# Performance work log

Hardware: AMD Instinct MI355X
Metric: run time of the kernel (lower is better)

## Reference

```python
import jax, jax.numpy as jnp
import numpy as np

DELTA = 1e-6  # small constant used throughout the original repo


def _theta(memory, keys):
    # batchwise cosine similarity: memory [b,m,w], keys [b,r,w] -> [b,r,m]
    a = memory / (jnp.linalg.norm(memory, axis=2, keepdims=True) + DELTA)
    b = keys / (jnp.linalg.norm(keys, axis=2, keepdims=True) + DELTA)
    return jnp.einsum('bmw,brw->brm', a, b)


def _content_weightings(memory, keys, strengths):
    d = _theta(memory, keys)                       # [b,r,m]
    s = jax.nn.softplus(strengths)[..., None]      # [b,r,1]
    return jax.nn.softmax(d * s, axis=2)


def _allocate(usage):
    # usage [b,m]
    u = DELTA + (1.0 - DELTA) * usage
    phi = jnp.argsort(u, axis=1)                          # ascending, like topk(largest=False)
    sorted_u = jnp.take_along_axis(u, phi, axis=1)
    sorted_alloc = (1.0 - sorted_u) * jnp.cumprod(sorted_u, axis=1)  # fake_cumprod == inclusive cumprod
    alloc = jnp.take_along_axis(sorted_alloc, phi, axis=1)           # faithful to .gather(1, phi) in source
    return alloc[:, None, :]                              # [b,1,m]


def _dnc_step(xi, W, bW, memory, link_matrix, precedence, read_weights, write_weights, usage_vector):
    b, m, w = memory.shape
    r = read_weights.shape[1]
    iface = xi @ W + bW                                   # [b, r*w + 3*w + 5*r + 3]
    i0 = r * w
    read_keys = iface[:, :i0].reshape(b, r, w)
    read_strengths = 1.0 + jax.nn.relu(iface[:, i0:i0 + r])              # [b,r]
    write_key = iface[:, i0 + r:i0 + r + w].reshape(b, 1, w)
    write_strength = (1.0 + jax.nn.relu(iface[:, i0 + r + w]))[:, None]  # [b,1]
    erase_vector = jax.nn.sigmoid(iface[:, i0 + r + w + 1:i0 + r + 2 * w + 1]).reshape(b, 1, w)
    write_vector = iface[:, i0 + r + 2 * w + 1:i0 + r + 3 * w + 1].reshape(b, 1, w)
    free_gates = jax.nn.sigmoid(iface[:, i0 + r + 3 * w + 1:i0 + 2 * r + 3 * w + 1])  # [b,r]
    allocation_gate = jax.nn.sigmoid(iface[:, i0 + 2 * r + 3 * w + 1])[:, None]       # [b,1]
    write_gate = jax.nn.sigmoid(iface[:, i0 + 2 * r + 3 * w + 2])[:, None]            # [b,1]
    # NOTE: source slices read_modes starting at the write_gate index (faithful) and softmaxes over dim 1
    read_modes = jax.nn.softmax(iface[:, i0 + 2 * r + 3 * w + 2:i0 + 5 * r + 3 * w + 2].reshape(b, r, 3), axis=1)

    # ---- write path ----
    usage = usage_vector + (1.0 - usage_vector) * (1.0 - jnp.prod(1.0 - write_weights, axis=1))
    psi = jnp.prod(1.0 - free_gates[:, :, None] * read_weights, axis=1)  # [b,m]
    usage = usage * psi

    write_content_w = _content_weightings(memory, write_key, write_strength)  # [b,1,m]
    alloc = _allocate(usage)                                                  # [b,1,m]
    ag = allocation_gate[:, :, None]
    wg = write_gate[:, :, None]
    new_write_w = wg * (ag * alloc + (1.0 - ag) * write_content_w)            # [b,1,m]

    weighted_resets = new_write_w[:, :, :, None] * erase_vector[:, :, None, :]  # [b,1,m,w]
    reset_gate = jnp.prod(1.0 - weighted_resets, axis=1)                        # [b,m,w]
    new_memory = memory * reset_gate + jnp.einsum('bkm,bkw->bmw', new_write_w, write_vector)

    prec4 = precedence[:, :, None, :]            # [b,1,1,m]
    ww_i = new_write_w[:, :, :, None]            # [b,1,m,1]
    ww_j = new_write_w[:, :, None, :]            # [b,1,1,m]
    new_link = (1.0 - ww_i - ww_j) * link_matrix + ww_i * prec4
    new_link = new_link * (1.0 - jnp.eye(m, dtype=memory.dtype))[None, None]

    new_prec = (1.0 - jnp.sum(new_write_w, axis=2, keepdims=True)) * precedence + new_write_w

    # ---- read path ----
    content_w = _content_weightings(new_memory, read_keys, read_strengths)  # [b,r,m]
    forward_w = jnp.einsum('bkmn,brn->brkm', new_link, read_weights)        # [b,r,1,m]
    backward_w = jnp.einsum('brm,bkmn->brkn', read_weights, new_link)       # [b,r,1,m]
    content_mode = read_modes[:, :, 2:3] * content_w
    backward_mode = jnp.sum(read_modes[:, :, 0:1, None] * backward_w, axis=2)
    forward_mode = jnp.sum(read_modes[:, :, 1:2, None] * forward_w, axis=2)
    new_read_w = backward_mode + content_mode + forward_mode                # [b,r,m]

    read_vectors = jnp.einsum('brm,bmw->brw', new_read_w, new_memory)       # [b,r,w]
    return read_vectors


def setup_inputs() -> dict:
    key = jax.random.key(0)
    ks = jax.random.split(key, 3)
    b, m, w, r, d = 64, 1024, 64, 4, 512
    iface_size = r * w + 3 * w + 5 * r + 3  # 471
    return {
        'xi': jax.random.normal(ks[0], (b, d), dtype=jnp.float32),
        'W': jax.random.normal(ks[1], (d, iface_size), dtype=jnp.float32) * 0.05,
        'bW': jnp.zeros((iface_size,), dtype=jnp.float32),
        'memory': jnp.zeros((b, m, w), dtype=jnp.float32),
        'link_matrix': jnp.zeros((b, 1, m, m), dtype=jnp.float32),
        'precedence': jnp.zeros((b, 1, m), dtype=jnp.float32),
        'read_weights': jnp.zeros((b, r, m), dtype=jnp.float32),
        'write_weights': jnp.zeros((b, 1, m), dtype=jnp.float32),
        'usage_vector': jnp.zeros((b, m), dtype=jnp.float32),
    }


def reference(xi, W, bW, memory, link_matrix, precedence, read_weights, write_weights, usage_vector):
    return _dnc_step(xi, W, bW, memory, link_matrix, precedence, read_weights, write_weights, usage_vector)
```

## Files before the change

### kernel.cpp

```cpp
#include <hip/hip_runtime.h>

#define DELTA 1e-6f

#define NB 64
#define NM 1024
#define NW 64
#define NR 4
#define ND 512
#define NIF 471

typedef unsigned long long ull;

__device__ __forceinline__ float sigmoidf_(float x){ return 1.0f/(1.0f+expf(-x)); }
__device__ __forceinline__ float softplusf_(float x){ return fmaxf(x,0.0f) + log1pf(expf(-fabsf(x))); }

__device__ __forceinline__ float waveSum(float v){
  #pragma unroll
  for(int o=32;o>0;o>>=1) v += __shfl_down(v,o,64);
  return v;
}
__device__ __forceinline__ float waveMax(float v){
  #pragma unroll
  for(int o=32;o>0;o>>=1) v = fmaxf(v, __shfl_down(v,o,64));
  return v;
}
__device__ __forceinline__ ull shflxor64(ull k, int m){
  unsigned lo = (unsigned)(k & 0xffffffffu), hi = (unsigned)(k>>32);
  lo = (unsigned)__shfl_xor((int)lo, m, 64);
  hi = (unsigned)__shfl_xor((int)hi, m, 64);
  return ((ull)hi<<32)|lo;
}

__global__ __launch_bounds__(256) void k_zero(float4* __restrict__ p, int n4){
  int i = blockIdx.x*256 + threadIdx.x;
  if (i < n4) p[i] = make_float4(0.f,0.f,0.f,0.f);
}

__global__ __launch_bounds__(256) void k_iface(const float* __restrict__ xi,
                                               const float* __restrict__ Wm,
                                               const float* __restrict__ bW,
                                               float* __restrict__ iface){
  int b = blockIdx.x, half = blockIdx.y;
  __shared__ float xs[ND];
  for(int k=threadIdx.x;k<ND;k+=256) xs[k]=xi[b*ND+k];
  __syncthreads();
  int c = half*236 + threadIdx.x;
  int cend = half ? NIF : 236;
  if (c < cend){
    float acc = bW[c];
    #pragma unroll 4
    for(int k=0;k<ND;k++) acc = fmaf(xs[k], Wm[k*NIF+c], acc);
    iface[b*NIF+c]=acc;
  }
}

__global__ __launch_bounds__(256) void k_wcos(
    const float* __restrict__ iface, const float* __restrict__ mem,
    const float* __restrict__ rw_old, const float* __restrict__ ww_old,
    const float* __restrict__ uv,
    float* __restrict__ uu, float* __restrict__ wcd, float* __restrict__ wcn){
  int b = blockIdx.y;
  int j = blockIdx.x*256 + threadIdx.x;
  __shared__ float wkey[NW];
  const float* ifb = iface + b*NIF;
  if (threadIdx.x < NW) wkey[threadIdx.x] = ifb[260+threadIdx.x];
  __syncthreads();
  float fg0=sigmoidf_(ifb[453]), fg1=sigmoidf_(ifb[454]);
  float fg2=sigmoidf_(ifb[455]), fg3=sigmoidf_(ifb[456]);
  float u0  = uv[b*NM+j];
  float wwo = ww_old[b*NM+j];
  float usage = u0 + (1.0f-u0)*wwo;
  float psi = (1.0f - fg0*rw_old[(b*NR+0)*NM+j])
            * (1.0f - fg1*rw_old[(b*NR+1)*NM+j])
            * (1.0f - fg2*rw_old[(b*NR+2)*NM+j])
            * (1.0f - fg3*rw_old[(b*NR+3)*NM+j]);
  usage *= psi;
  uu[b*NM+j] = DELTA + (1.0f-DELTA)*usage;
  float dot=0.0f, nrm=0.0f;
  const float4* mrow4 = (const float4*)(mem + ((size_t)b*NM + j)*NW);
  #pragma unroll 4
  for(int k=0;k<16;k++){
    float4 mv = mrow4[k];
    const float* wk = wkey + k*4;
    dot = fmaf(mv.x,wk[0],dot); dot = fmaf(mv.y,wk[1],dot);
    dot = fmaf(mv.z,wk[2],dot); dot = fmaf(mv.w,wk[3],dot);
    nrm = fmaf(mv.x,mv.x,nrm); nrm = fmaf(mv.y,mv.y,nrm);
    nrm = fmaf(mv.z,mv.z,nrm); nrm = fmaf(mv.w,mv.w,nrm);
  }
  wcd[b*NM+j]=dot; wcn[b*NM+j]=nrm;
}

__global__ __launch_bounds__(1024) void k_write2(
    const float* __restrict__ iface, const float* __restrict__ uu,
    const float* __restrict__ wcd, const float* __restrict__ wcn,
    float* __restrict__ wwp){
  int b = blockIdx.x; int tid = threadIdx.x;
  int lane = tid & 63, wv = tid >> 6;
  __shared__ float wkey[NW];
  __shared__ ull skA[NM];
  __shared__ ull skB[NM];
  __shared__ float fb2[NM];
  __shared__ float red[17];
  __shared__ float s_wp[16], s_wp2[16];
  const float* ifb = iface + b*NIF;
  if (tid < NW) wkey[tid] = ifb[260+tid];
  __syncthreads();
  float sw = softplusf_(1.0f + fmaxf(ifb[324],0.0f));
  float ag = sigmoidf_(ifb[457]);
  float wg = sigmoidf_(ifb[458]);
  float kn=0.0f;
  for(int k=0;k<NW;k++){ float t=wkey[k]; kn += t*t; }
  kn = sqrtf(kn);
  float logit = sw * wcd[b*NM+tid] / ((sqrtf(wcn[b*NM+tid])+DELTA)*(kn+DELTA));
  float m1 = waveMax(logit); if(lane==0) red[wv]=m1; __syncthreads();
  if(tid==0){ float mm=red[0]; for(int i=1;i<16;i++) mm=fmaxf(mm,red[i]); red[16]=mm; } __syncthreads();
  float e = expf(logit - red[16]);
  float s1 = waveSum(e); if(lane==0) red[wv]=s1; __syncthreads();
  if(tid==0){ float ss=0; for(int i=0;i<16;i++) ss+=red[i]; red[16]=ss; } __syncthreads();
  float wcw = e/red[16];
  float u = uu[b*NM+tid];
  ull k = ((ull)__float_as_uint(u) << 32) | (unsigned)tid;
  bool useA = true;
  for (int k2=2; k2<=NM; k2<<=1){
    for (int jj=k2>>1; jj>0; jj>>=1){
      ull p;
      if (jj >= 64){
        ull* buf = useA ? skA : skB;
        buf[tid] = k;
        __syncthreads();
        p = buf[tid^jj];
        useA = !useA;
      } else {
        p = shflxor64(k, jj);
      }
      bool lower = (tid & jj) == 0;
      bool asc   = (tid & k2) == 0;
      bool takeMin = (lower == asc);
      k = takeMin ? (k<p ? k : p) : (k>p ? k : p);
    }
  }
  float su = __uint_as_float((unsigned)(k>>32));
  int phi  = (int)(k & 0xffffffffu);
  float sc = su;
  #pragma unroll
  for (int off=1; off<64; off<<=1){
    float t = __shfl_up(sc, off, 64);
    if (lane >= off) sc *= t;
  }
  if (lane==63) s_wp[wv] = sc;
  __syncthreads();
  if (tid==0){
    float p=1.0f;
    for (int w=0;w<16;w++){ float t=s_wp[w]; s_wp2[w]=p; p*=t; }
  }
  __syncthreads();
  float P = sc * s_wp2[wv];
  float salloc = (1.0f - su)*P;
  fb2[phi] = salloc;
  __syncthreads();
  float alloc = fb2[tid];
  wwp[b*NM+tid] = wg*(ag*alloc + (1.0f-ag)*wcw);
}

__global__ __launch_bounds__(256) void k_link6(
    const float* __restrict__ link, const float* __restrict__ rw,
    const float* __restrict__ wwp,
    float* __restrict__ RFp, float* __restrict__ C2p, float* __restrict__ C3p,
    float* __restrict__ ldiag){
  int cx = blockIdx.x, ry = blockIdx.y, b = blockIdx.z;
  int tid = threadIdx.x, lane = tid&63, wv = tid>>6;
  __shared__ float4 s_L4[32*64];
  __shared__ float4 s_gcol4[256];
  __shared__ float  s_mwc[256];
  __shared__ float4 s_grow4[32];
  __shared__ float  s_wwr[32];
  __shared__ float4 s_rfp4[128];
  const float* Lb = link + ((size_t)b<<20);
  int colbase = cx*256, rowbase = ry*256;
  {
    float g0 = rw[(b*NR+0)*NM + colbase + tid];
    float g1 = rw[(b*NR+1)*NM + colbase + tid];
    float g2 = rw[(b*NR+2)*NM + colbase + tid];
    float g3 = rw[(b*NR+3)*NM + colbase + tid];
    s_gcol4[tid] = make_float4(g0,g1,g2,g3);
    s_mwc[tid] = 1.0f - wwp[b*NM + colbase + tid];
  }
  float c2a[NR][4], c3a[NR][4];
  #pragma unroll
  for(int r=0;r<NR;r++){
    #pragma unroll
    for(int e=0;e<4;e++){ c2a[r][e]=0.0f; c3a[r][e]=0.0f; }
  }
  for (int ch=0; ch<8; ++ch){
    int rb = rowbase + ch*32;
    if (tid < 128) ((float*)s_grow4)[tid] = rw[(b*NR+(tid&3))*NM + rb + (tid>>2)];
    if (tid < 32)  s_wwr[tid] = wwp[b*NM + rb + tid];
    #pragma unroll
    for (int jq=0;jq<8;jq++){
      int rl = wv + 4*jq;
      float4 lv = *(const float4*)(Lb + (size_t)(rb+rl)*NM + colbase + lane*4);
      s_L4[rl*64 + (lane ^ (rl&7))] = lv;
    }
    __syncthreads();
    if (cx == ry && tid < 32){
      int coff = ch*32 + tid;
      float4 v = s_L4[tid*64 + ((coff>>2) ^ (tid&7))];
      float d = (coff&1) ? ((coff&2)? v.w : v.y) : ((coff&2)? v.z : v.x);
      ldiag[b*NM + rb + tid] = d;
    }
    {
      int row = lane&31, h = lane>>5, row7 = row&7;
      float wwj = s_wwr[row];
      float rf[4] = {0,0,0,0};
      #pragma unroll 2
      for (int i=0;i<8;i++){
        int cb = wv*16 + h*8 + i;
        float4 lv = s_L4[row*64 + (cb ^ row7)];
        float4 mw = ((const float4*)s_mwc)[cb];
        float le[4] = {lv.x,lv.y,lv.z,lv.w};
        float mv[4] = {mw.x,mw.y,mw.z,mw.w};
        #pragma unroll
        for (int e=0;e<4;e++){
          float4 gv = s_gcol4[cb*4+e];
          float ls = le[e]*(mv[e]-wwj);
          rf[0] = fmaf(ls, gv.x, rf[0]);
          rf[1] = fmaf(ls, gv.y, rf[1]);
          rf[2] = fmaf(ls, gv.z, rf[2]);
          rf[3] = fmaf(ls, gv.w, rf[3]);
        }
      }
      #pragma unroll
      for (int r=0;r<NR;r++) rf[r] += __shfl_xor(rf[r], 32, 64);
      if (lane < 32) s_rfp4[wv*32+row] = make_float4(rf[0],rf[1],rf[2],rf[3]);
    }
    #pragma unroll 2
    for (int ri=0; ri<8; ri++){
      int row = wv*8 + ri;
      float4 lv = s_L4[row*64 + (lane ^ (row&7))];
      float4 gg = s_grow4[row];
      float wwr = s_wwr[row];
      float le[4] = {lv.x,lv.y,lv.z,lv.w};
      float ggv[4] = {gg.x,gg.y,gg.z,gg.w};
      float ggw[4];
      #pragma unroll
      for (int r=0;r<NR;r++) ggw[r] = ggv[r]*wwr;
      #pragma unroll
      for (int e=0;e<4;e++){
        #pragma unroll
        for (int r=0;r<NR;r++){
          c2a[r][e] = fmaf(le[e], ggv[r], c2a[r][e]);
          c3a[r][e] = fmaf(le[e], ggw[r], c3a[r][e]);
        }
      }
    }
    __syncthreads();
    if (tid < 128){
      int row = tid>>2, r = tid&3;
      float s = ((const float*)&s_rfp4[0*32+row])[r] + ((const float*)&s_rfp4[1*32+row])[r]
              + ((const float*)&s_rfp4[2*32+row])[r] + ((const float*)&s_rfp4[3*32+row])[r];
      RFp[((size_t)cx<<18) + (b*NR+r)*NM + rb + row] = s;
    }
  }
  __syncthreads();
  float4* s_comb = s_L4;
  #pragma unroll
  for (int r=0;r<NR;r++){
    s_comb[(wv*64+lane)*8 + r]     = make_float4(c2a[r][0],c2a[r][1],c2a[r][2],c2a[r][3]);
    s_comb[(wv*64+lane)*8 + 4 + r] = make_float4(c3a[r][0],c3a[r][1],c3a[r][2],c3a[r][3]);
  }
  __syncthreads();
  for (int t=tid; t<512; t+=256){
    int lc = t>>3, q = t&7;
    float4 a = s_comb[(0*64+lc)*8+q];
    float4 bb= s_comb[(1*64+lc)*8+q];
    float4 c = s_comb[(2*64+lc)*8+q];
    float4 d = s_comb[(3*64+lc)*8+q];
    float4 s = make_float4(a.x+bb.x+c.x+d.x, a.y+bb.y+c.y+d.y, a.z+bb.z+c.z+d.z, a.w+bb.w+c.w+d.w);
    float* dst = (q<4) ? &C2p[((size_t)ry<<18) + (b*NR+q)*NM + colbase + lc*4]
                       : &C3p[((size_t)ry<<18) + (b*NR+(q-4))*NM + colbase + lc*4];
    *(float4*)dst = s;
  }
}

__global__ __launch_bounds__(256) void k_comb(
    const float* __restrict__ RFp, const float* __restrict__ C2p, const float* __restrict__ C3p,
    float* __restrict__ RF, float* __restrict__ C2, float* __restrict__ C3){
  int idx = blockIdx.x*256 + threadIdx.x;
  RF[idx] = RFp[idx] + RFp[(1<<18)+idx] + RFp[(2<<18)+idx] + RFp[(3<<18)+idx];
  C2[idx] = C2p[idx] + C2p[(1<<18)+idx] + C2p[(2<<18)+idx] + C2p[(3<<18)+idx];
  C3[idx] = C3p[idx] + C3p[(1<<18)+idx] + C3p[(2<<18)+idx] + C3p[(3<<18)+idx];
}

__global__ __launch_bounds__(256) void k_rdots(
    const float* __restrict__ iface, const float* __restrict__ mem,
    const float* __restrict__ wwp, float* __restrict__ dots){
  int b = blockIdx.y;
  int j = blockIdx.x*256 + threadIdx.x;
  __shared__ float keys[NR][NW];
  __shared__ float er[NW], wvec[NW];
  const float* ifb = iface + b*NIF;
  { int r=threadIdx.x>>6, kk=threadIdx.x&63; keys[r][kk] = ifb[r*NW+kk]; }
  if (threadIdx.x < 64) er[threadIdx.x] = sigmoidf_(ifb[325+threadIdx.x]);
  else if (threadIdx.x < 128) wvec[threadIdx.x-64] = ifb[389+threadIdx.x-64];
  __syncthreads();
  float wwj = wwp[b*NM+j];
  const float* mrow = mem + ((size_t)b*NM+j)*NW;
  float dt[NR]={0,0,0,0}; float nrm=0.0f;
  for(int k=0;k<NW;k++){
    float nmv = fmaf(mrow[k], (1.0f - wwj*er[k]), wwj*wvec[k]);
    nrm = fmaf(nmv,nmv,nrm);
    #pragma unroll
    for(int r=0;r<NR;r++) dt[r] = fmaf(nmv, keys[r][k], dt[r]);
  }
  #pragma unroll
  for(int r=0;r<NR;r++) dots[(b*5+r)*NM + j] = dt[r];
  dots[(b*5+4)*NM + j] = nrm;
}

__global__ __launch_bounds__(1024) void k_rmid(
    const float* __restrict__ iface, const float* __restrict__ prec,
    const float* __restrict__ rw_old, const float* __restrict__ wwp,
    const float* __restrict__ dots, const float* __restrict__ ldiag,
    const float* __restrict__ RF, const float* __restrict__ C2, const float* __restrict__ C3,
    float* __restrict__ nrwg){
  int b = blockIdx.x; int tid = threadIdx.x; int lane=tid&63, wv=tid>>6;
  __shared__ float s_pk[16][8];
  __shared__ float scal[16];
  __shared__ float smax[NR], ssum[NR];
  __shared__ float rm[NR][3];
  const float* ifb = iface + b*NIF;
  if (tid == 0){
    for(int mo=0;mo<3;mo++){
      float x0=ifb[458+0*3+mo], x1=ifb[458+1*3+mo], x2=ifb[458+2*3+mo], x3=ifb[458+3*3+mo];
      float mx = fmaxf(fmaxf(x0,x1),fmaxf(x2,x3));
      float e0=expf(x0-mx),e1=expf(x1-mx),e2=expf(x2-mx),e3=expf(x3-mx);
      float s=e0+e1+e2+e3;
      rm[0][mo]=e0/s; rm[1][mo]=e1/s; rm[2][mo]=e2/s; rm[3][mo]=e3/s;
    }
  }
  if (tid >= 320 && tid < 324){
    int r = tid-320;
    float knv=0;
    for(int k=0;k<NW;k++){ float t=ifb[r*NW+k]; knv += t*t; }
    scal[8+r]  = sqrtf(knv);
    scal[12+r] = softplusf_(1.0f + fmaxf(ifb[256+r],0.0f));
  }
  __syncthreads();
  int j = tid;
  float pj  = prec[b*NM+j];
  float wwj = wwp[b*NM+j];
  float rwv[NR];
  #pragma unroll
  for(int r=0;r<NR;r++) rwv[r]=rw_old[(b*NR+r)*NM+j];
  {
    float v8[8];
    #pragma unroll
    for(int r=0;r<NR;r++){ v8[r] = pj*rwv[r]; v8[4+r] = wwj*rwv[r]; }
    #pragma unroll
    for(int q=0;q<8;q++){
      float s = waveSum(v8[q]);
      if(lane==0) s_pk[wv][q]=s;
    }
    __syncthreads();
    if (tid < 8){
      float ss=0;
      for(int w=0;w<16;w++) ss += s_pk[w][tid];
      scal[tid]=ss;
    }
    __syncthreads();
  }
  float dt[NR];
  #pragma unroll
  for(int r=0;r<NR;r++) dt[r] = dots[(b*5+r)*NM + j];
  float nrm = dots[(b*5+4)*NM + j];
  float inv = 1.0f/(sqrtf(nrm)+DELTA);
  float logit[NR], ce[NR], cw[NR];
  #pragma unroll
  for(int r=0;r<NR;r++) logit[r] = scal[12+r]*dt[r]*inv/(scal[8+r]+DELTA);
  #pragma unroll
  for(int r=0;r<NR;r++){
    float m1 = waveMax(logit[r]);
    if(lane==0) s_pk[wv][r]=m1;
  }
  __syncthreads();
  if (tid < NR){
    float mm=s_pk[0][tid];
    for(int w=1;w<16;w++) mm=fmaxf(mm,s_pk[w][tid]);
    smax[tid]=mm;
  }
  __syncthreads();
  #pragma unroll
  for(int r=0;r<NR;r++){
    ce[r] = expf(logit[r]-smax[r]);
    float s1 = waveSum(ce[r]);
    if(lane==0) s_pk[wv][r]=s1;
  }
  __syncthreads();
  if (tid < NR){
    float ss=0;
    for(int w=0;w<16;w++) ss += s_pk[w][tid];
    ssum[tid]=ss;
  }
  __syncthreads();
  #pragma unroll
  for(int r=0;r<NR;r++) cw[r] = ce[r]/ssum[r];
  float Ljj = ldiag[b*NM+j];
  #pragma unroll
  for(int r=0;r<NR;r++){
    float F   = RF[(b*NR+r)*NM+j];
    float cc2 = C2[(b*NR+r)*NM+j], cc3 = C3[(b*NR+r)*NM+j];
    float grj = rwv[r];
    float fwd = F - Ljj*grj*(1.0f-2.0f*wwj) + wwj*(scal[r] - pj*grj);
    float bwd = (cc2 - cc3) - Ljj*grj*(1.0f-wwj) - wwj*(cc2 - Ljj*grj) + pj*(scal[4+r] - wwj*grj);
    nrwg[(b*NR+r)*NM+j] = rm[r][0]*bwd + rm[r][1]*fwd + rm[r][2]*cw[r];
  }
}

__global__ __launch_bounds__(256) void k_readb(
    const float* __restrict__ iface, const float* __restrict__ mem,
    const float* __restrict__ wwp, const float* __restrict__ nrwg,
    float* __restrict__ out){
  int jt = blockIdx.x, b = blockIdx.y;
  int tid = threadIdx.x, lane = tid&63, wv = tid>>6;
  __shared__ float s_nrw[NR][256];
  __shared__ float s_ww[256];
  __shared__ float s_er[NW], s_wv[NW];
  __shared__ float s_acc[4][NR][NW];
  const float* ifb = iface + b*NIF;
  int j0 = jt*256;
  #pragma unroll
  for(int r=0;r<NR;r++) s_nrw[r][tid] = nrwg[(b*NR+r)*NM + j0+tid];
  s_ww[tid] = wwp[b*NM + j0+tid];
  if (tid < 64) s_er[tid] = sigmoidf_(ifb[325+tid]);
  else if (tid < 128) s_wv[tid-64] = ifb[389+tid-64];
  __syncthreads();
  int w = lane;
  float erw = s_er[w], wvw = s_wv[w];
  float acc[NR]={0,0,0,0};
  for(int jj=0;jj<64;jj++){
    int jl = wv*64+jj;
    float wwr = s_ww[jl];
    float nmv = fmaf(mem[((size_t)b*NM + j0+jl)*NW + w], (1.0f - wwr*erw), wwr*wvw);
    #pragma unroll
    for(int r=0;r<NR;r++) acc[r] = fmaf(s_nrw[r][jl], nmv, acc[r]);
  }
  #pragma unroll
  for(int r=0;r<NR;r++) s_acc[wv][r][w] = acc[r];
  __syncthreads();
  {
    int r = tid>>6, k = tid&63;
    float s = s_acc[0][r][k]+s_acc[1][r][k]+s_acc[2][r][k]+s_acc[3][r][k];
    atomicAdd(&out[b*NR*NW + r*NW + k], s);
  }
}

extern "C" void kernel_launch(void* const* d_in, const int* in_sizes, int n_in,
                              void* d_out, int out_size, void* d_ws, size_t ws_size,
                              hipStream_t stream) {
  (void)in_sizes; (void)n_in; (void)out_size; (void)ws_size;
  const float* xi   = (const float*)d_in[0];
  const float* Wm   = (const float*)d_in[1];
  const float* bW   = (const float*)d_in[2];
  const float* mem  = (const float*)d_in[3];
  const float* link = (const float*)d_in[4];
  const float* prec = (const float*)d_in[5];
  const float* rw   = (const float*)d_in[6];
  const float* wwo  = (const float*)d_in[7];
  const float* uv   = (const float*)d_in[8];
  float* out = (float*)d_out;
  float* ws  = (float*)d_ws;
  float* iface = ws;
  float* wwp   = ws + 30208;
  float* uu    = ws + 95744;
  float* wcd   = ws + 161280;
  float* wcn   = ws + 226816;
  float* dots  = ws + 292352;
  float* ldiag = ws + 620032;
  float* nrwg  = ws + 685568;
  float* RF    = ws + 947712;
  float* C2    = ws + 1209856;
  float* C3    = ws + 1472000;
  float* RFp   = ws + 1734144;
  float* C2p   = ws + 2782720;
  float* C3p   = ws + 3831296;
  k_zero <<<16, 256, 0, stream>>>((float4*)out, 4096);
  k_iface<<<dim3(NB,2), 256, 0, stream>>>(xi, Wm, bW, iface);
  k_wcos <<<dim3(4,NB), 256, 0, stream>>>(iface, mem, rw, wwo, uv, uu, wcd, wcn);
  k_write2<<<NB, 1024, 0, stream>>>(iface, uu, wcd, wcn, wwp);
  k_link6<<<dim3(4,4,NB), 256, 0, stream>>>(link, rw, wwp, RFp, C2p, C3p, ldiag);
  k_comb <<<1024, 256, 0, stream>>>(RFp, C2p, C3p, RF, C2, C3);
  k_rdots<<<dim3(4,NB), 256, 0, stream>>>(iface, mem, wwp, dots);
  k_rmid <<<NB, 1024, 0, stream>>>(iface, prec, rw, wwp, dots, ldiag, RF, C2, C3, nrwg);
  k_readb<<<dim3(4,NB), 256, 0, stream>>>(iface, mem, wwp, nrwg, out);
}
```

Baseline: 162.3 us.

## Stream link rows directly into registers and reduce row sums with DPP

The link-matrix kernel stops staging 32-row chunks through LDS with per-chunk barriers. Each wave now streams 64 rows straight from global memory into registers, with the column read-weights and 1-ww held in registers. The row-wise forward sums are reduced across the wave with DPP and xor shuffles, and the partial sums are stored as float4 per row so the combine and mid kernels read them vectorised. This removes the LDS round trips and barriers in the main loop, at the cost of a long shuffle reduction chain on every row and more register pressure.

Result: slower. 204.7 us (+26.1%).

```diff
diff --git a/kernel.cpp b/kernel.cpp
--- a/kernel.cpp
+++ b/kernel.cpp
@@ -29,6 +29,14 @@
   lo = (unsigned)__shfl_xor((int)lo, m, 64);
   hi = (unsigned)__shfl_xor((int)hi, m, 64);
   return ((ull)hi<<32)|lo;
+}
+__device__ __forceinline__ float dpp_xor1(float x){
+  int p = __builtin_amdgcn_update_dpp(0, __float_as_int(x), 0xB1, 0xF, 0xF, true);
+  return __int_as_float(p);
+}
+__device__ __forceinline__ float dpp_xor2(float x){
+  int p = __builtin_amdgcn_update_dpp(0, __float_as_int(x), 0x4E, 0xF, 0xF, true);
+  return __int_as_float(p);
 }
 
 __global__ __launch_bounds__(256) void k_zero(float4* __restrict__ p, int n4){
@@ -162,111 +170,94 @@
   wwp[b*NM+tid] = wg*(ag*alloc + (1.0f-ag)*wcw);
 }
 
-__global__ __launch_bounds__(256) void k_link6(
+__global__ __launch_bounds__(256) void k_link7(
     const float* __restrict__ link, const float* __restrict__ rw,
     const float* __restrict__ wwp,
-    float* __restrict__ RFp, float* __restrict__ C2p, float* __restrict__ C3p,
+    float4* __restrict__ RFp, float* __restrict__ C2p, float* __restrict__ C3p,
     float* __restrict__ ldiag){
   int cx = blockIdx.x, ry = blockIdx.y, b = blockIdx.z;
   int tid = threadIdx.x, lane = tid&63, wv = tid>>6;
-  __shared__ float4 s_L4[32*64];
-  __shared__ float4 s_gcol4[256];
-  __shared__ float  s_mwc[256];
-  __shared__ float4 s_grow4[32];
-  __shared__ float  s_wwr[32];
-  __shared__ float4 s_rfp4[128];
+  __shared__ float4 s_grow4[256];
+  __shared__ float  s_wwr[256];
+  __shared__ float4 s_rf4[256];
+  __shared__ float4 s_comb[2048];
+  int colbase = cx*256, rowbase = ry*256;
+  for (int t=tid; t<1024; t+=256)
+    ((float*)s_grow4)[t] = rw[(b*NR+(t&3))*NM + rowbase + (t>>2)];
+  s_wwr[tid] = wwp[b*NM + rowbase + tid];
+  int c0 = colbase + lane*4;
+  float g[NR][4], mwc[4];
+  {
+    float4 wwc4 = *(const float4*)(wwp + b*NM + c0);
+    mwc[0]=1.0f-wwc4.x; mwc[1]=1.0f-wwc4.y; mwc[2]=1.0f-wwc4.z; mwc[3]=1.0f-wwc4.w;
+    #pragma unroll
+    for (int r=0;r<NR;r++){
+      float4 gv = *(const float4*)(rw + (b*NR+r)*NM + c0);
+      g[r][0]=gv.x; g[r][1]=gv.y; g[r][2]=gv.z; g[r][3]=gv.w;
+    }
+  }
+  float c2a[NR][4], c3a[NR][4];
+  #pragma unroll
+  for(int r=0;r<NR;r++){
+    #pragma unroll
+    for(int e=0;e<4;e++){ c2a[r][e]=0.0f; c3a[r][e]=0.0f; }
+  }
+  __syncthreads();
   const float* Lb = link + ((size_t)b<<20);
-  int colbase = cx*256, rowbase = ry*256;
-  {
-    float g0 = rw[(b*NR+0)*NM + colbase + tid];
-    float g1 = rw[(b*NR+1)*NM + colbase + tid];
-    float g2 = rw[(b*NR+2)*NM + colbase + tid];
-    float g3 = rw[(b*NR+3)*NM + colbase + tid];
-    s_gcol4[tid] = make_float4(g0,g1,g2,g3);
-    s_mwc[tid] = 1.0f - wwp[b*NM + colbase + tid];
-  }
-  float c2a[NR][4], c3a[NR][4];
-  #pragma unroll
-  for(int r=0;r<NR;r++){
-    #pragma unroll
-    for(int e=0;e<4;e++){ c2a[r][e]=0.0f; c3a[r][e]=0.0f; }
-  }
-  for (int ch=0; ch<8; ++ch){
-    int rb = rowbase + ch*32;
-    if (tid < 128) ((float*)s_grow4)[tid] = rw[(b*NR+(tid&3))*NM + rb + (tid>>2)];
-    if (tid < 32)  s_wwr[tid] = wwp[b*NM + rb + tid];
-    #pragma unroll
-    for (int jq=0;jq<8;jq++){
-      int rl = wv + 4*jq;
-      float4 lv = *(const float4*)(Lb + (size_t)(rb+rl)*NM + colbase + lane*4);
-      s_L4[rl*64 + (lane ^ (rl&7))] = lv;
-    }
-    __syncthreads();
-    if (cx == ry && tid < 32){
-      int coff = ch*32 + tid;
-      float4 v = s_L4[tid*64 + ((coff>>2) ^ (tid&7))];
-      float d = (coff&1) ? ((coff&2)? v.w : v.y) : ((coff&2)? v.z : v.x);
-      ldiag[b*NM + rb + tid] = d;
-    }
-    {
-      int row = lane&31, h = lane>>5, row7 = row&7;
-      float wwj = s_wwr[row];
-      float rf[4] = {0,0,0,0};
-      #pragma unroll 2
-      for (int i=0;i<8;i++){
-        int cb = wv*16 + h*8 + i;
-        float4 lv = s_L4[row*64 + (cb ^ row7)];
-        float4 mw = ((const float4*)s_mwc)[cb];
-        float le[4] = {lv.x,lv.y,lv.z,lv.w};
-        float mv[4] = {mw.x,mw.y,mw.z,mw.w};
-        #pragma unroll
-        for (int e=0;e<4;e++){
-          float4 gv = s_gcol4[cb*4+e];
-          float ls = le[e]*(mv[e]-wwj);
-          rf[0] = fmaf(ls, gv.x, rf[0]);
-          rf[1] = fmaf(ls, gv.y, rf[1]);
-          rf[2] = fmaf(ls, gv.z, rf[2]);
-          rf[3] = fmaf(ls, gv.w, rf[3]);
-        }
+  const bool isdiag = (cx==ry);
+  int rowlo = wv*64;
+  #pragma unroll 2
+  for (int i=0;i<64;i++){
+    int rl = rowlo + i;
+    const float4 lv = *(const float4*)(Lb + (size_t)(rowbase+rl)*NM + c0);
+    float le[4] = {lv.x, lv.y, lv.z, lv.w};
+    float wwj = s_wwr[rl];
+    float4 gr = s_grow4[rl];
+    float grv[4] = {gr.x, gr.y, gr.z, gr.w};
+    float gw[4];
+    #pragma unroll
+    for (int r=0;r<NR;r++) gw[r] = grv[r]*wwj;
+    float p0=0.f,p1=0.f,p2=0.f,p3=0.f;
+    #pragma unroll
+    for (int e=0;e<4;e++){
+      #pragma unroll
+      for (int r=0;r<NR;r++){
+        c2a[r][e] = fmaf(le[e], grv[r], c2a[r][e]);
+        c3a[r][e] = fmaf(le[e], gw[r],  c3a[r][e]);
       }
-      #pragma unroll
-      for (int r=0;r<NR;r++) rf[r] += __shfl_xor(rf[r], 32, 64);
-      if (lane < 32) s_rfp4[wv*32+row] = make_float4(rf[0],rf[1],rf[2],rf[3]);
-    }
-    #pragma unroll 2
-    for (int ri=0; ri<8; ri++){
-      int row = wv*8 + ri;
-      float4 lv = s_L4[row*64 + (lane ^ (row&7))];
-      float4 gg = s_grow4[row];
-      float wwr = s_wwr[row];
-      float le[4] = {lv.x,lv.y,lv.z,lv.w};
-      float ggv[4] = {gg.x,gg.y,gg.z,gg.w};
-      float ggw[4];
-      #pragma unroll
-      for (int r=0;r<NR;r++) ggw[r] = ggv[r]*wwr;
-      #pragma unroll
-      for (int e=0;e<4;e++){
-        #pragma unroll
-        for (int r=0;r<NR;r++){
-          c2a[r][e] = fmaf(le[e], ggv[r], c2a[r][e]);
-          c3a[r][e] = fmaf(le[e], ggw[r], c3a[r][e]);
-        }
+      float lt = le[e]*(mwc[e]-wwj);
+      p0 = fmaf(lt, g[0][e], p0);
+      p1 = fmaf(lt, g[1][e], p1);
+      p2 = fmaf(lt, g[2][e], p2);
+      p3 = fmaf(lt, g[3][e], p3);
+    }
+    float s0 = p0 + dpp_xor1(p0);
+    float s1 = p1 + dpp_xor1(p1);
+    float s2 = p2 + dpp_xor1(p2);
+    float s3 = p3 + dpp_xor1(p3);
+    float wa = (lane&1)? s1 : s0;
+    float wb = (lane&1)? s3 : s2;
+    wa += dpp_xor2(wa);
+    wb += dpp_xor2(wb);
+    float w = (lane&2)? wb : wa;
+    w += __shfl_xor(w, 4, 64);
+    w += __shfl_xor(w, 8, 64);
+    w += __shfl_xor(w, 16, 64);
+    w += __shfl_xor(w, 32, 64);
+    if (lane < 4) ((float*)s_rf4)[rl*4 + lane] = w;
+    if (isdiag){
+      if ((rl>>2) == lane){
+        float dv = (rl&1) ? ((rl&2)? le[3] : le[1]) : ((rl&2)? le[2] : le[0]);
+        ldiag[b*NM + rowbase + rl] = dv;
       }
     }
-    __syncthreads();
-    if (tid < 128){
-      int row = tid>>2, r = tid&3;
-      float s = ((const float*)&s_rfp4[0*32+row])[r] + ((const float*)&s_rfp4[1*32+row])[r]
-              + ((const float*)&s_rfp4[2*32+row])[r] + ((const float*)&s_rfp4[3*32+row])[r];
-      RFp[((size_t)cx<<18) + (b*NR+r)*NM + rb + row] = s;
-    }
-  }
-  __syncthreads();
-  float4* s_comb = s_L4;
+  }
+  __syncthreads();
+  RFp[((size_t)cx<<16) + b*NM + rowbase + tid] = s_rf4[tid];
   #pragma unroll
   for (int r=0;r<NR;r++){
-    s_comb[(wv*64+lane)*8 + r]     = make_float4(c2a[r][0],c2a[r][1],c2a[r][2],c2a[r][3]);
-    s_comb[(wv*64+lane)*8 + 4 + r] = make_float4(c3a[r][0],c3a[r][1],c3a[r][2],c3a[r][3]);
+    s_comb[tid*8 + r]     = make_float4(c2a[r][0],c2a[r][1],c2a[r][2],c2a[r][3]);
+    s_comb[tid*8 + 4 + r] = make_float4(c3a[r][0],c3a[r][1],c3a[r][2],c3a[r][3]);
   }
   __syncthreads();
   for (int t=tid; t<512; t+=256){
@@ -283,12 +274,15 @@
 }
 
 __global__ __launch_bounds__(256) void k_comb(
-    const float* __restrict__ RFp, const float* __restrict__ C2p, const float* __restrict__ C3p,
-    float* __restrict__ RF, float* __restrict__ C2, float* __restrict__ C3){
+    const float4* __restrict__ RFp4, const float* __restrict__ C2p, const float* __restrict__ C3p,
+    float4* __restrict__ RF4, float* __restrict__ C2, float* __restrict__ C3){
   int idx = blockIdx.x*256 + threadIdx.x;
-  RF[idx] = RFp[idx] + RFp[(1<<18)+idx] + RFp[(2<<18)+idx] + RFp[(3<<18)+idx];
-  C2[idx] = C2p[idx] + C2p[(1<<18)+idx] + C2p[(2<<18)+idx] + C2p[(3<<18)+idx];
-  C3[idx] = C3p[idx] + C3p[(1<<18)+idx] + C3p[(2<<18)+idx] + C3p[(3<<18)+idx];
+  if (idx < 65536){
+    float4 a=RFp4[idx], b=RFp4[65536+idx], c=RFp4[131072+idx], d=RFp4[196608+idx];
+    RF4[idx] = make_float4(a.x+b.x+c.x+d.x, a.y+b.y+c.y+d.y, a.z+b.z+c.z+d.z, a.w+b.w+c.w+d.w);
+  }
+  C2[idx] = C2p[idx] + C2p[262144+idx] + C2p[524288+idx] + C2p[786432+idx];
+  C3[idx] = C3p[idx] + C3p[262144+idx] + C3p[524288+idx] + C3p[786432+idx];
 }
 
 __global__ __launch_bounds__(256) void k_rdots(
@@ -321,7 +315,7 @@
     const float* __restrict__ iface, const float* __restrict__ prec,
     const float* __restrict__ rw_old, const float* __restrict__ wwp,
     const float* __restrict__ dots, const float* __restrict__ ldiag,
-    const float* __restrict__ RF, const float* __restrict__ C2, const float* __restrict__ C3,
+    const float4* __restrict__ RF4, const float* __restrict__ C2, const float* __restrict__ C3,
     float* __restrict__ nrwg){
   int b = blockIdx.x; int tid = threadIdx.x; int lane=tid&63, wv=tid>>6;
   __shared__ float s_pk[16][8];
@@ -405,9 +399,11 @@
   #pragma unroll
   for(int r=0;r<NR;r++) cw[r] = ce[r]/ssum[r];
   float Ljj = ldiag[b*NM+j];
+  float4 Fv = RF4[b*NM + j];
+  float Fr[4] = {Fv.x, Fv.y, Fv.z, Fv.w};
   #pragma unroll
   for(int r=0;r<NR;r++){
-    float F   = RF[(b*NR+r)*NM+j];
+    float F   = Fr[r];
     float cc2 = C2[(b*NR+r)*NM+j], cc3 = C3[(b*NR+r)*NM+j];
     float grj = rwv[r];
     float fwd = F - Ljj*grj*(1.0f-2.0f*wwj) + wwj*(scal[r] - pj*grj);
@@ -487,9 +483,9 @@
   k_iface<<<dim3(NB,2), 256, 0, stream>>>(xi, Wm, bW, iface);
   k_wcos <<<dim3(4,NB), 256, 0, stream>>>(iface, mem, rw, wwo, uv, uu, wcd, wcn);
   k_write2<<<NB, 1024, 0, stream>>>(iface, uu, wcd, wcn, wwp);
-  k_link6<<<dim3(4,4,NB), 256, 0, stream>>>(link, rw, wwp, RFp, C2p, C3p, ldiag);
-  k_comb <<<1024, 256, 0, stream>>>(RFp, C2p, C3p, RF, C2, C3);
+  k_link7<<<dim3(4,4,NB), 256, 0, stream>>>(link, rw, wwp, (float4*)RFp, C2p, C3p, ldiag);
+  k_comb <<<1024, 256, 0, stream>>>((const float4*)RFp, C2p, C3p, (float4*)RF, C2, C3);
   k_rdots<<<dim3(4,NB), 256, 0, stream>>>(iface, mem, wwp, dots);
-  k_rmid <<<NB, 1024, 0, stream>>>(iface, prec, rw, wwp, dots, ldiag, RF, C2, C3, nrwg);
+  k_rmid <<<NB, 1024, 0, stream>>>(iface, prec, rw, wwp, dots, ldiag, (const float4*)RF, C2, C3, nrwg);
   k_readb<<<dim3(4,NB), 256, 0, stream>>>(iface, mem, wwp, nrwg, out);
 }
```

## Fold partial-sum combine into k_rmid and retile link forward-reduction loop

Applied to the files above, without the earlier changes.

Removes the separate k_comb kernel. Its four-way sum of column/row-block partials is now done directly in k_rmid, and the RF partials are stored in an interleaved float4 layout so each lane reads them with one vector load. Inside k_link the forward-term loop now gives each lane two rows and a 4-column group, reduced with two xor shuffles. The shared-memory swizzle changes to (row>>1)&7 to keep bank conflicts low for the new access pattern. In exchange, k_rmid does more global loads, and a __syncthreads per chunk is added.

Result: faster. 158.6 us (-2.3%).

```diff
diff --git a/kernel.cpp b/kernel.cpp
--- a/kernel.cpp
+++ b/kernel.cpp
@@ -162,10 +162,10 @@
   wwp[b*NM+tid] = wg*(ag*alloc + (1.0f-ag)*wcw);
 }
 
-__global__ __launch_bounds__(256) void k_link6(
+__global__ __launch_bounds__(256) void k_link8(
     const float* __restrict__ link, const float* __restrict__ rw,
     const float* __restrict__ wwp,
-    float* __restrict__ RFp, float* __restrict__ C2p, float* __restrict__ C3p,
+    float4* __restrict__ RFp, float* __restrict__ C2p, float* __restrict__ C3p,
     float* __restrict__ ldiag){
   int cx = blockIdx.x, ry = blockIdx.y, b = blockIdx.z;
   int tid = threadIdx.x, lane = tid&63, wv = tid>>6;
@@ -199,44 +199,57 @@
     for (int jq=0;jq<8;jq++){
       int rl = wv + 4*jq;
       float4 lv = *(const float4*)(Lb + (size_t)(rb+rl)*NM + colbase + lane*4);
-      s_L4[rl*64 + (lane ^ (rl&7))] = lv;
+      s_L4[rl*64 + (lane ^ ((rl>>1)&7))] = lv;
     }
     __syncthreads();
     if (cx == ry && tid < 32){
       int coff = ch*32 + tid;
-      float4 v = s_L4[tid*64 + ((coff>>2) ^ (tid&7))];
+      float4 v = s_L4[tid*64 + ((coff>>2) ^ ((tid>>1)&7))];
       float d = (coff&1) ? ((coff&2)? v.w : v.y) : ((coff&2)? v.z : v.x);
       ldiag[b*NM + rb + tid] = d;
     }
     {
-      int row = lane&31, h = lane>>5, row7 = row&7;
-      float wwj = s_wwr[row];
-      float rf[4] = {0,0,0,0};
-      #pragma unroll 2
-      for (int i=0;i<8;i++){
-        int cb = wv*16 + h*8 + i;
-        float4 lv = s_L4[row*64 + (cb ^ row7)];
-        float4 mw = ((const float4*)s_mwc)[cb];
-        float le[4] = {lv.x,lv.y,lv.z,lv.w};
-        float mv[4] = {mw.x,mw.y,mw.z,mw.w};
+      int i5 = lane & 15, cg = lane >> 4;
+      int rl0 = 2*i5;
+      int sz = i5 & 7;
+      float wwj0 = s_wwr[rl0], wwj1 = s_wwr[rl0+1];
+      float rf0[4] = {0,0,0,0}, rf1[4] = {0,0,0,0};
+      #pragma unroll
+      for (int q=0;q<4;q++){
+        int cq = wv*16 + cg*4 + q;
+        float4 mw  = ((const float4*)s_mwc)[cq];
+        float4 lv0 = s_L4[rl0*64 + (cq ^ sz)];
+        float4 lv1 = s_L4[(rl0+1)*64 + (cq ^ sz)];
+        float le0[4]={lv0.x,lv0.y,lv0.z,lv0.w};
+        float le1[4]={lv1.x,lv1.y,lv1.z,lv1.w};
+        float mv[4]={mw.x,mw.y,mw.z,mw.w};
         #pragma unroll
         for (int e=0;e<4;e++){
-          float4 gv = s_gcol4[cb*4+e];
-          float ls = le[e]*(mv[e]-wwj);
-          rf[0] = fmaf(ls, gv.x, rf[0]);
-          rf[1] = fmaf(ls, gv.y, rf[1]);
-          rf[2] = fmaf(ls, gv.z, rf[2]);
-          rf[3] = fmaf(ls, gv.w, rf[3]);
+          float4 gv = s_gcol4[cq*4+e];
+          float lt0 = le0[e]*(mv[e]-wwj0);
+          float lt1 = le1[e]*(mv[e]-wwj1);
+          rf0[0]=fmaf(lt0,gv.x,rf0[0]); rf0[1]=fmaf(lt0,gv.y,rf0[1]);
+          rf0[2]=fmaf(lt0,gv.z,rf0[2]); rf0[3]=fmaf(lt0,gv.w,rf0[3]);
+          rf1[0]=fmaf(lt1,gv.x,rf1[0]); rf1[1]=fmaf(lt1,gv.y,rf1[1]);
+          rf1[2]=fmaf(lt1,gv.z,rf1[2]); rf1[3]=fmaf(lt1,gv.w,rf1[3]);
         }
       }
       #pragma unroll
-      for (int r=0;r<NR;r++) rf[r] += __shfl_xor(rf[r], 32, 64);
-      if (lane < 32) s_rfp4[wv*32+row] = make_float4(rf[0],rf[1],rf[2],rf[3]);
+      for (int r=0;r<NR;r++){
+        rf0[r] += __shfl_xor(rf0[r], 16, 64);
+        rf0[r] += __shfl_xor(rf0[r], 32, 64);
+        rf1[r] += __shfl_xor(rf1[r], 16, 64);
+        rf1[r] += __shfl_xor(rf1[r], 32, 64);
+      }
+      if (cg == 0){
+        s_rfp4[wv*32 + rl0]     = make_float4(rf0[0],rf0[1],rf0[2],rf0[3]);
+        s_rfp4[wv*32 + rl0 + 1] = make_float4(rf1[0],rf1[1],rf1[2],rf1[3]);
+      }
     }
     #pragma unroll 2
     for (int ri=0; ri<8; ri++){
       int row = wv*8 + ri;
-      float4 lv = s_L4[row*64 + (lane ^ (row&7))];
+      float4 lv = s_L4[row*64 + (lane ^ ((row>>1)&7))];
       float4 gg = s_grow4[row];
       float wwr = s_wwr[row];
       float le[4] = {lv.x,lv.y,lv.z,lv.w};
@@ -258,15 +271,15 @@
       int row = tid>>2, r = tid&3;
       float s = ((const float*)&s_rfp4[0*32+row])[r] + ((const float*)&s_rfp4[1*32+row])[r]
               + ((const float*)&s_rfp4[2*32+row])[r] + ((const float*)&s_rfp4[3*32+row])[r];
-      RFp[((size_t)cx<<18) + (b*NR+r)*NM + rb + row] = s;
-    }
-  }
-  __syncthreads();
+      ((float*)RFp)[((size_t)cx<<18) + (b*NM + rb + row)*4 + r] = s;
+    }
+    __syncthreads();
+  }
   float4* s_comb = s_L4;
   #pragma unroll
   for (int r=0;r<NR;r++){
-    s_comb[(wv*64+lane)*8 + r]     = make_float4(c2a[r][0],c2a[r][1],c2a[r][2],c2a[r][3]);
-    s_comb[(wv*64+lane)*8 + 4 + r] = make_float4(c3a[r][0],c3a[r][1],c3a[r][2],c3a[r][3]);
+    s_comb[tid*8 + r]     = make_float4(c2a[r][0],c2a[r][1],c2a[r][2],c2a[r][3]);
+    s_comb[tid*8 + 4 + r] = make_float4(c3a[r][0],c3a[r][1],c3a[r][2],c3a[r][3]);
   }
   __syncthreads();
   for (int t=tid; t<512; t+=256){
@@ -280,15 +293,6 @@
                        : &C3p[((size_t)ry<<18) + (b*NR+(q-4))*NM + colbase + lc*4];
     *(float4*)dst = s;
   }
-}
-
-__global__ __launch_bounds__(256) void k_comb(
-    const float* __restrict__ RFp, const float* __restrict__ C2p, const float* __restrict__ C3p,
-    float* __restrict__ RF, float* __restrict__ C2, float* __restrict__ C3){
-  int idx = blockIdx.x*256 + threadIdx.x;
-  RF[idx] = RFp[idx] + RFp[(1<<18)+idx] + RFp[(2<<18)+idx] + RFp[(3<<18)+idx];
-  C2[idx] = C2p[idx] + C2p[(1<<18)+idx] + C2p[(2<<18)+idx] + C2p[(3<<18)+idx];
-  C3[idx] = C3p[idx] + C3p[(1<<18)+idx] + C3p[(2<<18)+idx] + C3p[(3<<18)+idx];
 }
 
 __global__ __launch_bounds__(256) void k_rdots(
@@ -321,7 +325,7 @@
     const float* __restrict__ iface, const float* __restrict__ prec,
     const float* __restrict__ rw_old, const float* __restrict__ wwp,
     const float* __restrict__ dots, const float* __restrict__ ldiag,
-    const float* __restrict__ RF, const float* __restrict__ C2, const float* __restrict__ C3,
+    const float4* __restrict__ RFp4, const float* __restrict__ C2p, const float* __restrict__ C3p,
     float* __restrict__ nrwg){
   int b = blockIdx.x; int tid = threadIdx.x; int lane=tid&63, wv=tid>>6;
   __shared__ float s_pk[16][8];
@@ -405,10 +409,18 @@
   #pragma unroll
   for(int r=0;r<NR;r++) cw[r] = ce[r]/ssum[r];
   float Ljj = ldiag[b*NM+j];
+  float4 Fa = RFp4[(0<<16) + b*NM + j];
+  float4 Fb = RFp4[(1<<16) + b*NM + j];
+  float4 Fc = RFp4[(2<<16) + b*NM + j];
+  float4 Fd = RFp4[(3<<16) + b*NM + j];
+  float Fr[4] = {Fa.x+Fb.x+Fc.x+Fd.x, Fa.y+Fb.y+Fc.y+Fd.y,
+                 Fa.z+Fb.z+Fc.z+Fd.z, Fa.w+Fb.w+Fc.w+Fd.w};
   #pragma unroll
   for(int r=0;r<NR;r++){
-    float F   = RF[(b*NR+r)*NM+j];
-    float cc2 = C2[(b*NR+r)*NM+j], cc3 = C3[(b*NR+r)*NM+j];
+    int idx = (b*NR+r)*NM + j;
+    float cc2 = C2p[idx] + C2p[262144+idx] + C2p[524288+idx] + C2p[786432+idx];
+    float cc3 = C3p[idx] + C3p[262144+idx] + C3p[524288+idx] + C3p[786432+idx];
+    float F   = Fr[r];
     float grj = rwv[r];
     float fwd = F - Ljj*grj*(1.0f-2.0f*wwj) + wwj*(scal[r] - pj*grj);
     float bwd = (cc2 - cc3) - Ljj*grj*(1.0f-wwj) - wwj*(cc2 - Ljj*grj) + pj*(scal[4+r] - wwj*grj);
@@ -477,19 +489,15 @@
   float* dots  = ws + 292352;
   float* ldiag = ws + 620032;
   float* nrwg  = ws + 685568;
-  float* RF    = ws + 947712;
-  float* C2    = ws + 1209856;
-  float* C3    = ws + 1472000;
-  float* RFp   = ws + 1734144;
-  float* C2p   = ws + 2782720;
-  float* C3p   = ws + 3831296;
+  float* RFp   = ws + 947712;
+  float* C2p   = ws + 1996288;
+  float* C3p   = ws + 3044864;
   k_zero <<<16, 256, 0, stream>>>((float4*)out, 4096);
   k_iface<<<dim3(NB,2), 256, 0, stream>>>(xi, Wm, bW, iface);
   k_wcos <<<dim3(4,NB), 256, 0, stream>>>(iface, mem, rw, wwo, uv, uu, wcd, wcn);
   k_write2<<<NB, 1024, 0, stream>>>(iface, uu, wcd, wcn, wwp);
-  k_link6<<<dim3(4,4,NB), 256, 0, stream>>>(link, rw, wwp, RFp, C2p, C3p, ldiag);
-  k_comb <<<1024, 256, 0, stream>>>(RFp, C2p, C3p, RF, C2, C3);
+  k_link8<<<dim3(4,4,NB), 256, 0, stream>>>(link, rw, wwp, (float4*)RFp, C2p, C3p, ldiag);
   k_rdots<<<dim3(4,NB), 256, 0, stream>>>(iface, mem, wwp, dots);
-  k_rmid <<<NB, 1024, 0, stream>>>(iface, prec, rw, wwp, dots, ldiag, RF, C2, C3, nrwg);
+  k_rmid <<<NB, 1024, 0, stream>>>(iface, prec, rw, wwp, dots, ldiag, (const float4*)RFp, C2p, C3p, nrwg);
   k_readb<<<dim3(4,NB), 256, 0, stream>>>(iface, mem, wwp, nrwg, out);
 }
```
